# Performance work log

Measured on AMD Instinct MI355X. Metric: run time of the kernel, lower is better.

Reference implementation:

```python
import jax, jax.numpy as jnp
import numpy as np

N, E, D = 50000, 600000, 128

def _lin(key, fan_in, fan_out):
    kw, kb = jax.random.split(key)
    s = 1.0 / np.sqrt(fan_in)
    W = jax.random.uniform(kw, (fan_in, fan_out), minval=-s, maxval=s, dtype=jnp.float32)
    b = jax.random.uniform(kb, (fan_out,), minval=-s, maxval=s, dtype=jnp.float32)
    return W, b

def setup_inputs() -> dict:
    key = jax.random.key(0)
    ks = jax.random.split(key, 16)
    h = jax.random.normal(ks[0], (N, D), dtype=jnp.float32)
    pos = jax.random.normal(ks[1], (N, 2), dtype=jnp.float32)
    edge_index = jax.random.randint(ks[2], (2, E), 0, N, dtype=jnp.int64)
    edge_attr = jax.random.uniform(ks[3], (E, 1), dtype=jnp.float32)
    Wq, bq = _lin(ks[4], D, D)
    Wk, bk = _lin(ks[5], D, D)
    Wv, bv = _lin(ks[6], D, D)
    We1, be1 = _lin(ks[7], 1, D)
    We2, be2 = _lin(ks[8], D, D)
    Wa1, ba1 = _lin(ks[9], 3 * D, D)
    Wa2, ba2 = _lin(ks[10], D, 1)
    Wm1, bm1 = _lin(ks[11], 2 * D, D)
    Wm2, bm2 = _lin(ks[12], D, D)
    return dict(h=h, pos=pos, edge_index=edge_index, edge_attr=edge_attr,
                Wq=Wq, bq=bq, Wk=Wk, bk=bk, Wv=Wv, bv=bv,
                We1=We1, be1=be1, We2=We2, be2=be2,
                Wa1=Wa1, ba1=ba1, Wa2=Wa2, ba2=ba2,
                Wm1=Wm1, bm1=bm1, Wm2=Wm2, bm2=bm2)

def reference(h, pos, edge_index, edge_attr,
              Wq, bq, Wk, bk, Wv, bv,
              We1, be1, We2, be2,
              Wa1, ba1, Wa2, ba2,
              Wm1, bm1, Wm2, bm2):
    row, col = edge_index[0], edge_index[1]  # source, destination
    q = h @ Wq + bq                          # [N, D]
    k = h @ Wk + bk
    v = h @ Wv + bv
    e = jax.nn.relu(edge_attr @ We1 + be1) @ We2 + be2  # [E, D]
    # per-edge attention logits
    attn_in = jnp.concatenate([q[col], k[row], e], axis=-1)          # [E, 3D]
    logits = (jax.nn.relu(attn_in @ Wa1 + ba1) @ Wa2 + ba2)[:, 0]    # [E]
    # segment softmax grouped by destination node (torch_geometric style)
    seg_max = jax.ops.segment_max(logits, col, num_segments=N)       # [N]
    ex = jnp.exp(logits - seg_max[col])
    seg_sum = jax.ops.segment_sum(ex, col, num_segments=N)           # [N]
    w = ex / (seg_sum[col] + 1e-16)                                  # [E]
    # per-edge messages
    msg_in = jnp.concatenate([v[row], e], axis=-1)                   # [E, 2D]
    msg = jax.nn.silu(msg_in @ Wm1 + bm1) @ Wm2 + bm2                # [E, D]
    agg = jax.ops.segment_sum(msg * w[:, None], col, num_segments=N) # [N, D]
    return (h + agg, pos)
```

## Files before the change

### kernel.cpp

```cpp
#include <hip/hip_runtime.h>
#include <math.h>

#define D 128
#define RPB 32
#define SB 256

typedef __attribute__((ext_vector_type(8))) short bf16x8;
typedef __attribute__((ext_vector_type(4))) float f32x4;

__device__ inline unsigned f2bf(float f) {
    unsigned u = __float_as_uint(f);
    return (u + 0x7FFFu + ((u >> 16) & 1u)) >> 16;
}

__global__ __launch_bounds__(128) void prep(
    const float* __restrict__ Wq, const float* __restrict__ bq,
    const float* __restrict__ Wk, const float* __restrict__ bk,
    const float* __restrict__ Wv, const float* __restrict__ bv,
    const float* __restrict__ Wa1, const float* __restrict__ ba1,
    const float* __restrict__ Wm1, const float* __restrict__ bm1,
    const float* __restrict__ We1, const float* __restrict__ be1,
    const float* __restrict__ We2, const float* __restrict__ be2,
    ushort* __restrict__ Wpk,
    float* __restrict__ bqa, float* __restrict__ bka, float* __restrict__ bva,
    float* __restrict__ bounds,
    float2* __restrict__ AB, float2* __restrict__ MB,
    int* __restrict__ deg, int N)
{
    int b = blockIdx.x;
    int j = threadIdx.x;
    if (b < 384) {
        int which = b >> 7, i = b & 127;
        const float *A, *B;
        if (which == 0)      { A = Wq; B = Wa1; }
        else if (which == 1) { A = Wk; B = Wa1 + 128 * D; }
        else                 { A = Wv; B = Wm1; }
        float acc = 0.f;
        for (int k = 0; k < D; k++) acc += A[i * D + k] * B[k * D + j];
        int gc = which * 128 + j;
        int nt = gc >> 4;
        int ks = i >> 5;
        int lane = (((i >> 3) & 3) << 4) | (gc & 15);
        int j8 = i & 7;
        Wpk[((nt * 4 + ks) * 64 + lane) * 8 + j8] = (ushort)f2bf(acc);
    } else if (b < 387) {
        int which = b - 384;
        const float *bias, *B, *extra; float *out;
        if (which == 0)      { bias = bq; B = Wa1;           out = bqa; extra = ba1; }
        else if (which == 1) { bias = bk; B = Wa1 + 128 * D; out = bka; extra = nullptr; }
        else                 { bias = bv; B = Wm1;           out = bva; extra = bm1; }
        float acc = extra ? extra[j] : 0.f;
        for (int k = 0; k < D; k++) acc += bias[k] * B[k * D + j];
        out[j] = acc;
    } else if (b == 387) {
        __shared__ float sb[128];
        float w = We1[j], bb = be1[j];
        float t = (w != 0.f) ? (-bb / w) : 2.f;
        t = fminf(fmaxf(t, 0.f), 1.f);
        sb[j] = t;
        __syncthreads();
        for (int k = 2; k <= 128; k <<= 1)
            for (int jj = k >> 1; jj > 0; jj >>= 1) {
                int ixj = j ^ jj;
                if (ixj > j) {
                    float a = sb[j], c = sb[ixj];
                    bool up = ((j & k) == 0);
                    if (up ? (a > c) : (a < c)) { sb[j] = c; sb[ixj] = a; }
                }
                __syncthreads();
            }
        if (j == 0) { bounds[0] = 0.f; bounds[129] = 1.f; }
        bounds[1 + j] = sb[j];
    } else if (b < 517) {
        __shared__ float sb[128];
        __shared__ float Ae[128], Be[128];
        float w = We1[j], bb = be1[j];
        float t = (w != 0.f) ? (-bb / w) : 2.f;
        t = fminf(fmaxf(t, 0.f), 1.f);
        sb[j] = t;
        __syncthreads();
        for (int k = 2; k <= 128; k <<= 1)
            for (int jj = k >> 1; jj > 0; jj >>= 1) {
                int ixj = j ^ jj;
                if (ixj > j) {
                    float a = sb[j], c = sb[ixj];
                    bool up = ((j & k) == 0);
                    if (up ? (a > c) : (a < c)) { sb[j] = c; sb[ixj] = a; }
                }
                __syncthreads();
            }
        int i = b - 388;
        float lo = (i == 0)   ? 0.f : sb[i - 1];
        float hi = (i == 128) ? 1.f : sb[i];
        float m = 0.5f * (lo + hi);
        float ae = 0.f, be = 0.f;
        for (int k = 0; k < 128; k++) {
            float ww = We1[k], bb2 = be1[k];
            if (m * ww + bb2 > 0.f) { ae += ww * We2[k * D + j]; be += bb2 * We2[k * D + j]; }
        }
        be += be2[j];
        Ae[j] = ae; Be[j] = be;
        __syncthreads();
        float aa = 0.f, ba = 0.f, am = 0.f, bm = 0.f;
        for (int l = 0; l < 128; l++) {
            float ael = Ae[l], bel = Be[l];
            float wa = Wa1[(256 + l) * D + j];
            float wm = Wm1[(128 + l) * D + j];
            aa += ael * wa; ba += bel * wa;
            am += ael * wm; bm += bel * wm;
        }
        AB[i * 128 + j] = make_float2(aa, ba);
        MB[i * 128 + j] = make_float2(am, bm);
    } else {
        int i = (b - 517) * 128 + j;
        if (i < N) deg[i] = 0;
    }
}

__global__ __launch_bounds__(256) void node_gemm(
    const float* __restrict__ h, int N,
    const ushort* __restrict__ Wpk,
    const float* __restrict__ bqa, const float* __restrict__ bka, const float* __restrict__ bva,
    float* __restrict__ qa, unsigned* __restrict__ kv)
{
    __shared__ __align__(16) ushort hsb[64 * 128];
    int t = threadIdx.x;
    int row0 = blockIdx.x * 64;
#pragma unroll
    for (int i = 0; i < 4; i++) {
        int g = t + i * 256;
        int r = g >> 4, c = g & 15;
        int grow = row0 + r;
        float4 f0, f1;
        if (grow < N) {
            const float4* hp = (const float4*)(h + (size_t)grow * D + c * 8);
            f0 = hp[0]; f1 = hp[1];
        } else {
            f0 = make_float4(0.f, 0.f, 0.f, 0.f); f1 = f0;
        }
        ushort u[8] = { (ushort)f2bf(f0.x), (ushort)f2bf(f0.y), (ushort)f2bf(f0.z), (ushort)f2bf(f0.w),
                        (ushort)f2bf(f1.x), (ushort)f2bf(f1.y), (ushort)f2bf(f1.z), (ushort)f2bf(f1.w) };
        int pc = c ^ (r & 15);
        *(uint4*)&hsb[r * 128 + pc * 8] = *(uint4*)u;
    }
    __syncthreads();

    int w = t >> 6, l = t & 63;
    int lrow = w * 16 + (l & 15);
    f32x4 acc[24];
#pragma unroll
    for (int i = 0; i < 24; i++) acc[i] = (f32x4){0.f, 0.f, 0.f, 0.f};

    const bf16x8* WB = (const bf16x8*)Wpk;
#pragma unroll
    for (int ks = 0; ks < 4; ks++) {
        int c = (ks * 4 + (l >> 4)) ^ (l & 15);
        bf16x8 afrag = *(const bf16x8*)&hsb[lrow * 128 + c * 8];
#pragma unroll
        for (int nt = 0; nt < 24; nt++) {
            bf16x8 bfrag = WB[(nt * 4 + ks) * 64 + l];
            acc[nt] = __builtin_amdgcn_mfma_f32_16x16x32_bf16(afrag, bfrag, acc[nt], 0, 0, 0);
        }
    }

    int rbase = row0 + w * 16 + ((l >> 4) << 2);
    int cl = l & 15;
#pragma unroll
    for (int cc = 0; cc < 8; cc++) {
        float bqv = bqa[cc * 16 + cl];
        float bkv = bka[cc * 16 + cl];
        float bvv = bva[cc * 16 + cl];
        f32x4 aq = acc[cc], ak = acc[8 + cc], av = acc[16 + cc];
#pragma unroll
        for (int r = 0; r < 4; r++) {
            int row = rbase + r;
            if (row < N) {
                qa[(size_t)row * D + cc * 16 + cl] = aq[r] + bqv;
                kv[(size_t)row * D + cc * 16 + cl] =
                    (f2bf(av[r] + bvv) << 16) | f2bf(ak[r] + bkv);
            }
        }
    }
}

__global__ __launch_bounds__(256) void k_hist(const int* __restrict__ ei, int E,
                                              int* __restrict__ deg)
{
    int e = blockIdx.x * 256 + threadIdx.x;
    if (e < E) atomicAdd(deg + ei[E + e], 1);
}

__global__ __launch_bounds__(SB) void k_scan1(const int* __restrict__ deg, int N,
                                              int* __restrict__ partial)
{
    __shared__ int ls[SB];
    int t = threadIdx.x;
    int i = blockIdx.x * SB + t;
    ls[t] = (i < N) ? deg[i] : 0;
    __syncthreads();
    for (int s = SB / 2; s > 0; s >>= 1) {
        if (t < s) ls[t] += ls[t + s];
        __syncthreads();
    }
    if (t == 0) partial[blockIdx.x] = ls[0];
}

__global__ __launch_bounds__(SB) void k_scan23(const int* __restrict__ deg, int N,
                                               const int* __restrict__ partial, int NB,
                                               int* __restrict__ off)
{
    __shared__ int lp[SB];
    __shared__ int ls[SB];
    int t = threadIdx.x;
    int pv = (t < NB) ? partial[t] : 0;
    lp[t] = pv;
    __syncthreads();
    int pval = pv;
    for (int s = 1; s < SB; s <<= 1) {
        int add = (t >= s) ? lp[t - s] : 0;
        __syncthreads();
        pval += add;
        lp[t] = pval;
        __syncthreads();
    }
    int base = (blockIdx.x > 0) ? lp[blockIdx.x - 1] : 0;

    int i = blockIdx.x * SB + t;
    int v = (i < N) ? deg[i] : 0;
    ls[t] = v;
    __syncthreads();
    int val = v;
    for (int s = 1; s < SB; s <<= 1) {
        int add = (t >= s) ? ls[t - s] : 0;
        __syncthreads();
        val += add;
        ls[t] = val;
        __syncthreads();
    }
    if (i < N) off[i] = base + val - v;
}

__global__ __launch_bounds__(256) void k_scatter(const int* __restrict__ ei,
                                                 const float* __restrict__ eattr, int E,
                                                 const float* __restrict__ bounds,
                                                 int* __restrict__ off, int2* __restrict__ recs)
{
    __shared__ float b[130];
    int t = threadIdx.x;
    if (t < 130) b[t] = bounds[t];
    __syncthreads();
    int e = blockIdx.x * 256 + t;
    if (e >= E) return;
    int row = ei[e], col = ei[E + e];
    float a = eattr[e];
    int lo = 0, hi = 128;
    while (lo < hi) { int mid = (lo + hi + 1) >> 1; if (b[mid] <= a) lo = mid; else hi = mid - 1; }
    int p = atomicAdd(off + col, 1);
    recs[p] = make_int2(row | (lo << 17), __float_as_int(a));
}

__global__ __launch_bounds__(256) void node_all(
    const int2* __restrict__ recs, int N,
    const int* __restrict__ off,
    const float* __restrict__ qa, const unsigned* __restrict__ kv,
    const float2* __restrict__ AB, const float2* __restrict__ MB,
    const float* __restrict__ Wa2, const float* __restrict__ ba2,
    float* __restrict__ S, float* __restrict__ segsum)
{
    int t = threadIdx.x;
    int lane = t & 63, wv = t >> 6;
    int l = lane & 31;
    int n = blockIdx.x * 8 + wv * 2 + (lane >> 5);
    bool valid = (n < N);
    int start = 0, end = 0;
    if (valid) {
        end = off[n];
        start = (n > 0) ? off[n - 1] : 0;
    }

    const char* kvc = (const char*)kv;
    const char* ABc = (const char*)AB;
    const char* MBc = (const char*)MB;

    float4 q4 = valid ? *(const float4*)(qa + (size_t)n * D + 4 * l)
                      : make_float4(0.f, 0.f, 0.f, 0.f);
    float4 w4 = *(const float4*)(Wa2 + 4 * l);
    float ba2v = ba2[0];

    float m_run = -INFINITY;
    float a0 = 0.f, a1 = 0.f, a2 = 0.f, a3 = 0.f, ssum = 0.f;

    for (int idx = start; idx < end; idx++) {
        int2 rec = recs[idx];
        unsigned w0 = (unsigned)rec.x;
        float a = __int_as_float(rec.y);
        int rowb = (int)(w0 & 0x1FFFFu) << 9;
        int tabb = (int)(w0 >> 17) << 10;

        uint4 kvp = *(const uint4*)(kvc + rowb + (l << 4));
        float4 ab0 = *(const float4*)(ABc + tabb + (l << 5));
        float4 ab1 = *(const float4*)(ABc + tabb + (l << 5) + 16);
        float4 mb0 = *(const float4*)(MBc + tabb + (l << 5));
        float4 mb1 = *(const float4*)(MBc + tabb + (l << 5) + 16);

        float k0 = __uint_as_float(kvp.x << 16);
        float v0 = __uint_as_float(kvp.x & 0xFFFF0000u);
        float k1 = __uint_as_float(kvp.y << 16);
        float v1 = __uint_as_float(kvp.y & 0xFFFF0000u);
        float k2 = __uint_as_float(kvp.z << 16);
        float v2 = __uint_as_float(kvp.z & 0xFFFF0000u);
        float k3 = __uint_as_float(kvp.w << 16);
        float v3 = __uint_as_float(kvp.w & 0xFFFF0000u);

        float part = fmaxf(q4.x + k0 + a * ab0.x + ab0.y, 0.f) * w4.x
                   + fmaxf(q4.y + k1 + a * ab0.z + ab0.w, 0.f) * w4.y
                   + fmaxf(q4.z + k2 + a * ab1.x + ab1.y, 0.f) * w4.z
                   + fmaxf(q4.w + k3 + a * ab1.z + ab1.w, 0.f) * w4.w;
#pragma unroll
        for (int s = 1; s < 32; s <<= 1) part += __shfl_xor(part, s, 64);
        float lg = part + ba2v;

        float mN = fmaxf(m_run, lg);
        float sc = __expf(m_run - mN);
        float ex = __expf(lg - mN);
        m_run = mN;

        float x0 = v0 + a * mb0.x + mb0.y;
        float x1 = v1 + a * mb0.z + mb0.w;
        float x2 = v2 + a * mb1.x + mb1.y;
        float x3 = v3 + a * mb1.z + mb1.w;
        float s0 = x0 * __builtin_amdgcn_rcpf(1.f + __expf(-x0));
        float s1 = x1 * __builtin_amdgcn_rcpf(1.f + __expf(-x1));
        float s2 = x2 * __builtin_amdgcn_rcpf(1.f + __expf(-x2));
        float s3 = x3 * __builtin_amdgcn_rcpf(1.f + __expf(-x3));

        a0 = a0 * sc + ex * s0;
        a1 = a1 * sc + ex * s1;
        a2 = a2 * sc + ex * s2;
        a3 = a3 * sc + ex * s3;
        ssum = ssum * sc + ex;
    }

    if (valid) {
        float inv = __builtin_amdgcn_rcpf(ssum + 1e-16f);
        *(float4*)(S + (size_t)n * D + 4 * l) =
            make_float4(a0 * inv, a1 * inv, a2 * inv, a3 * inv);
        if (l == 0) segsum[n] = ssum;
    }
}

__global__ __launch_bounds__(256) void node_out(
    const float* __restrict__ h, int N,
    const float* __restrict__ S, const float* __restrict__ Wm2, const float* __restrict__ bm2,
    const float* __restrict__ segsum, float* __restrict__ out,
    const float* __restrict__ pos, int npos, int G1)
{
    int b = blockIdx.x;
    if (b >= G1) {
        int i = ((b - G1) * 256 + threadIdx.x) * 4;
        float* outp = out + (size_t)N * D;
        if (i + 3 < npos) {
            *(float4*)(outp + i) = *(const float4*)(pos + i);
        } else {
            for (int j = i; j < npos; j++) outp[j] = pos[j];
        }
        return;
    }
    __shared__ float hsT[D][36];
    int r0 = b * RPB;
    int t = threadIdx.x;
    for (int x = t; x < RPB * D; x += 256) {
        int r = x >> 7, cc = x & 127;
        hsT[cc][r] = (r0 + r < N) ? S[(size_t)(r0 + r) * D + cc] : 0.f;
    }
    __syncthreads();
    int c = t & 127, half = t >> 7;
    float acc[16];
#pragma unroll
    for (int r = 0; r < 16; r++) acc[r] = 0.f;
    for (int k = 0; k < D; k++) {
        float w = Wm2[k * D + c];
        const float4* hp = (const float4*)&hsT[k][half * 16];
#pragma unroll
        for (int p = 0; p < 4; p++) {
            float4 hv = hp[p];
            acc[p * 4 + 0] += hv.x * w;
            acc[p * 4 + 1] += hv.y * w;
            acc[p * 4 + 2] += hv.z * w;
            acc[p * 4 + 3] += hv.w * w;
        }
    }
    float bb = bm2[c];
#pragma unroll
    for (int r = 0; r < 16; r++) {
        int row = r0 + half * 16 + r;
        if (row < N) {
            float ws = segsum[row];
            ws = ws / (ws + 1e-16f);
            out[(size_t)row * D + c] = h[(size_t)row * D + c] + acc[r] + bb * ws;
        }
    }
}

extern "C" void kernel_launch(void* const* d_in, const int* in_sizes, int n_in,
                              void* d_out, int out_size, void* d_ws, size_t ws_size,
                              hipStream_t stream)
{
    const float* h     = (const float*)d_in[0];
    const float* pos   = (const float*)d_in[1];
    const int*   ei    = (const int*)d_in[2];
    const float* eattr = (const float*)d_in[3];
    const float* Wq  = (const float*)d_in[4];  const float* bq  = (const float*)d_in[5];
    const float* Wk  = (const float*)d_in[6];  const float* bk  = (const float*)d_in[7];
    const float* Wv  = (const float*)d_in[8];  const float* bv  = (const float*)d_in[9];
    const float* We1 = (const float*)d_in[10]; const float* be1 = (const float*)d_in[11];
    const float* We2 = (const float*)d_in[12]; const float* be2 = (const float*)d_in[13];
    const float* Wa1 = (const float*)d_in[14]; const float* ba1 = (const float*)d_in[15];
    const float* Wa2 = (const float*)d_in[16]; const float* ba2 = (const float*)d_in[17];
    const float* Wm1 = (const float*)d_in[18]; const float* bm1 = (const float*)d_in[19];
    const float* Wm2 = (const float*)d_in[20]; const float* bm2 = (const float*)d_in[21];

    int N = in_sizes[0] / D;
    int E = in_sizes[3];
    int NB = (N + SB - 1) / SB;

    float* ws = (float*)d_ws;
    size_t off_f = 0;
    auto alloc = [&](size_t n) { float* p = ws + off_f; off_f += (n + 63) & ~(size_t)63; return p; };

    ushort* Wpk = (ushort*)alloc(24 * 4 * 64 * 8 / 2);
    float* bqa = alloc(D); float* bka = alloc(D); float* bva = alloc(D);
    float* bounds = alloc(130);
    float2* AB = (float2*)alloc((size_t)129 * 128 * 2);
    float2* MB = (float2*)alloc((size_t)129 * 128 * 2);
    float* qa = alloc((size_t)N * D);
    unsigned* kv = (unsigned*)alloc((size_t)N * D);
    float* S  = qa;
    float* segsum = alloc(N);
    int* deg  = (int*)alloc(N);
    int* offs = (int*)alloc(N);
    int* partial = (int*)alloc(256);
    int2* recs = (int2*)alloc((size_t)E * 2);

    int G0 = 517 + (N + 127) / 128;
    prep<<<G0, 128, 0, stream>>>(Wq, bq, Wk, bk, Wv, bv, Wa1, ba1, Wm1, bm1,
                                 We1, be1, We2, be2,
                                 Wpk, bqa, bka, bva, bounds, AB, MB, deg, N);

    k_hist<<<(E + 255) / 256, 256, 0, stream>>>(ei, E, deg);
    k_scan1<<<NB, SB, 0, stream>>>(deg, N, partial);
    k_scan23<<<NB, SB, 0, stream>>>(deg, N, partial, NB, offs);
    k_scatter<<<(E + 255) / 256, 256, 0, stream>>>(ei, eattr, E, bounds, offs, recs);

    node_gemm<<<(N + 63) / 64, 256, 0, stream>>>(h, N, Wpk, bqa, bka, bva, qa, kv);

    node_all<<<(N + 7) / 8, 256, 0, stream>>>(recs, N, offs, qa, kv, AB, MB,
                                              Wa2, ba2, S, segsum);

    int G1 = (N + RPB - 1) / RPB;
    int G2 = (2 * N + 1023) / 1024;
    node_out<<<G1 + G2, 256, 0, stream>>>(h, N, S, Wm2, bm2, segsum, (float*)d_out,
                                          pos, 2 * N, G1);
}
```

Before: 299.5 us.

## Fuse launches, unroll edge loop by two, MFMA bf16 output GEMM

Folds the degree histogram into the prep kernel (memset replaces zeroing) and merges the scatter and node GEMM into one launch, cutting kernel launches and letting independent work overlap. The per-node edge loop now handles two edges per iteration, rescales the running softmax max only when a logit jumps by more than 8, and drops the constant ba2 bias, which cancels in the softmax. The aggregated messages are stored as bf16, and the final Wm2 projection moves from a scalar fp32 loop to MFMA bf16 with a prepacked weight. This trades some precision in the output GEMM for fewer launches and less memory traffic.

After: 253.8 us. 1.18x faster.

```diff
diff --git a/kernel.cpp b/kernel.cpp
--- a/kernel.cpp
+++ b/kernel.cpp
@@ -2,7 +2,6 @@
 #include <math.h>
 
 #define D 128
-#define RPB 32
 #define SB 256
 
 typedef __attribute__((ext_vector_type(8))) short bf16x8;
@@ -21,11 +20,13 @@
     const float* __restrict__ Wm1, const float* __restrict__ bm1,
     const float* __restrict__ We1, const float* __restrict__ be1,
     const float* __restrict__ We2, const float* __restrict__ be2,
-    ushort* __restrict__ Wpk,
+    const float* __restrict__ Wm2,
+    const int* __restrict__ ei, int E,
+    ushort* __restrict__ Wpk, ushort* __restrict__ Wpk2,
     float* __restrict__ bqa, float* __restrict__ bka, float* __restrict__ bva,
     float* __restrict__ bounds,
     float2* __restrict__ AB, float2* __restrict__ MB,
-    int* __restrict__ deg, int N)
+    int* __restrict__ deg)
 {
     int b = blockIdx.x;
     int j = threadIdx.x;
@@ -111,21 +112,98 @@
         }
         AB[i * 128 + j] = make_float2(aa, ba);
         MB[i * 128 + j] = make_float2(am, bm);
+    } else if (b < 645) {
+        int i = b - 517;
+        int nt = j >> 4;
+        int ks = i >> 5;
+        int lane = (((i >> 3) & 3) << 4) | (j & 15);
+        int j8 = i & 7;
+        Wpk2[((nt * 4 + ks) * 64 + lane) * 8 + j8] = (ushort)f2bf(Wm2[i * D + j]);
     } else {
-        int i = (b - 517) * 128 + j;
-        if (i < N) deg[i] = 0;
-    }
-}
-
-__global__ __launch_bounds__(256) void node_gemm(
+        int e = (b - 645) * 128 + j;
+        if (e < E) atomicAdd(deg + ei[E + e], 1);
+    }
+}
+
+__global__ __launch_bounds__(SB) void k_scan1(const int* __restrict__ deg, int N,
+                                              int* __restrict__ partial)
+{
+    __shared__ int ls[SB];
+    int t = threadIdx.x;
+    int i = blockIdx.x * SB + t;
+    ls[t] = (i < N) ? deg[i] : 0;
+    __syncthreads();
+    for (int s = SB / 2; s > 0; s >>= 1) {
+        if (t < s) ls[t] += ls[t + s];
+        __syncthreads();
+    }
+    if (t == 0) partial[blockIdx.x] = ls[0];
+}
+
+__global__ __launch_bounds__(SB) void k_scan23(const int* __restrict__ deg, int N,
+                                               const int* __restrict__ partial, int NB,
+                                               int* __restrict__ off)
+{
+    __shared__ int lp[SB];
+    __shared__ int ls[SB];
+    int t = threadIdx.x;
+    int pv = (t < NB) ? partial[t] : 0;
+    lp[t] = pv;
+    __syncthreads();
+    int pval = pv;
+    for (int s = 1; s < SB; s <<= 1) {
+        int add = (t >= s) ? lp[t - s] : 0;
+        __syncthreads();
+        pval += add;
+        lp[t] = pval;
+        __syncthreads();
+    }
+    int base = (blockIdx.x > 0) ? lp[blockIdx.x - 1] : 0;
+
+    int i = blockIdx.x * SB + t;
+    int v = (i < N) ? deg[i] : 0;
+    ls[t] = v;
+    __syncthreads();
+    int val = v;
+    for (int s = 1; s < SB; s <<= 1) {
+        int add = (t >= s) ? ls[t - s] : 0;
+        __syncthreads();
+        val += add;
+        ls[t] = val;
+        __syncthreads();
+    }
+    if (i < N) off[i] = base + val - v;
+}
+
+__global__ __launch_bounds__(256) void scatter_gemm(
+    const int* __restrict__ ei, const float* __restrict__ eattr, int E,
+    const float* __restrict__ bounds, int* __restrict__ off, int2* __restrict__ recs,
+    int GS,
     const float* __restrict__ h, int N,
     const ushort* __restrict__ Wpk,
     const float* __restrict__ bqa, const float* __restrict__ bka, const float* __restrict__ bva,
     float* __restrict__ qa, unsigned* __restrict__ kv)
 {
     __shared__ __align__(16) ushort hsb[64 * 128];
+    __shared__ float bnd[130];
     int t = threadIdx.x;
-    int row0 = blockIdx.x * 64;
+    int blk = blockIdx.x;
+
+    if (blk < GS) {
+        if (t < 130) bnd[t] = bounds[t];
+        __syncthreads();
+        int e = blk * 256 + t;
+        if (e >= E) return;
+        int row = ei[e], col = ei[E + e];
+        float a = eattr[e];
+        int lo = 0, hi = 128;
+        while (lo < hi) { int mid = (lo + hi + 1) >> 1; if (bnd[mid] <= a) lo = mid; else hi = mid - 1; }
+        int p = atomicAdd(off + col, 1);
+        recs[p] = make_int2(row | (lo << 17), __float_as_int(a));
+        return;
+    }
+
+    int row0 = (blk - GS) * 64;
 #pragma unroll
     for (int i = 0; i < 4; i++) {
         int g = t + i * 256;
@@ -183,94 +261,17 @@
     }
 }
 
-__global__ __launch_bounds__(256) void k_hist(const int* __restrict__ ei, int E,
-                                              int* __restrict__ deg)
-{
-    int e = blockIdx.x * 256 + threadIdx.x;
-    if (e < E) atomicAdd(deg + ei[E + e], 1);
-}
-
-__global__ __launch_bounds__(SB) void k_scan1(const int* __restrict__ deg, int N,
-                                              int* __restrict__ partial)
-{
-    __shared__ int ls[SB];
-    int t = threadIdx.x;
-    int i = blockIdx.x * SB + t;
-    ls[t] = (i < N) ? deg[i] : 0;
-    __syncthreads();
-    for (int s = SB / 2; s > 0; s >>= 1) {
-        if (t < s) ls[t] += ls[t + s];
-        __syncthreads();
-    }
-    if (t == 0) partial[blockIdx.x] = ls[0];
-}
-
-__global__ __launch_bounds__(SB) void k_scan23(const int* __restrict__ deg, int N,
-                                               const int* __restrict__ partial, int NB,
-                                               int* __restrict__ off)
-{
-    __shared__ int lp[SB];
-    __shared__ int ls[SB];
-    int t = threadIdx.x;
-    int pv = (t < NB) ? partial[t] : 0;
-    lp[t] = pv;
-    __syncthreads();
-    int pval = pv;
-    for (int s = 1; s < SB; s <<= 1) {
-        int add = (t >= s) ? lp[t - s] : 0;
-        __syncthreads();
-        pval += add;
-        lp[t] = pval;
-        __syncthreads();
-    }
-    int base = (blockIdx.x > 0) ? lp[blockIdx.x - 1] : 0;
-
-    int i = blockIdx.x * SB + t;
-    int v = (i < N) ? deg[i] : 0;
-    ls[t] = v;
-    __syncthreads();
-    int val = v;
-    for (int s = 1; s < SB; s <<= 1) {
-        int add = (t >= s) ? ls[t - s] : 0;
-        __syncthreads();
-        val += add;
-        ls[t] = val;
-        __syncthreads();
-    }
-    if (i < N) off[i] = base + val - v;
-}
-
-__global__ __launch_bounds__(256) void k_scatter(const int* __restrict__ ei,
-                                                 const float* __restrict__ eattr, int E,
-                                                 const float* __restrict__ bounds,
-                                                 int* __restrict__ off, int2* __restrict__ recs)
-{
-    __shared__ float b[130];
-    int t = threadIdx.x;
-    if (t < 130) b[t] = bounds[t];
-    __syncthreads();
-    int e = blockIdx.x * 256 + t;
-    if (e >= E) return;
-    int row = ei[e], col = ei[E + e];
-    float a = eattr[e];
-    int lo = 0, hi = 128;
-    while (lo < hi) { int mid = (lo + hi + 1) >> 1; if (b[mid] <= a) lo = mid; else hi = mid - 1; }
-    int p = atomicAdd(off + col, 1);
-    recs[p] = make_int2(row | (lo << 17), __float_as_int(a));
-}
-
 __global__ __launch_bounds__(256) void node_all(
     const int2* __restrict__ recs, int N,
     const int* __restrict__ off,
     const float* __restrict__ qa, const unsigned* __restrict__ kv,
     const float2* __restrict__ AB, const float2* __restrict__ MB,
-    const float* __restrict__ Wa2, const float* __restrict__ ba2,
-    float* __restrict__ S, float* __restrict__ segsum)
+    const float* __restrict__ Wa2,
+    unsigned* __restrict__ Sb, float* __restrict__ segsum)
 {
     int t = threadIdx.x;
-    int lane = t & 63, wv = t >> 6;
-    int l = lane & 31;
-    int n = blockIdx.x * 8 + wv * 2 + (lane >> 5);
+    int l = t & 31;
+    int n = blockIdx.x * 8 + (t >> 5);
     bool valid = (n < N);
     int start = 0, end = 0;
     if (valid) {
@@ -285,79 +286,129 @@
     float4 q4 = valid ? *(const float4*)(qa + (size_t)n * D + 4 * l)
                       : make_float4(0.f, 0.f, 0.f, 0.f);
     float4 w4 = *(const float4*)(Wa2 + 4 * l);
-    float ba2v = ba2[0];
 
     float m_run = -INFINITY;
     float a0 = 0.f, a1 = 0.f, a2 = 0.f, a3 = 0.f, ssum = 0.f;
 
-    for (int idx = start; idx < end; idx++) {
+    int idx = start;
+    for (; idx + 2 <= end; idx += 2) {
+        int2 rec1 = recs[idx];
+        int2 rec2 = recs[idx + 1];
+        unsigned u1 = (unsigned)rec1.x, u2 = (unsigned)rec2.x;
+        float at1 = __int_as_float(rec1.y), at2 = __int_as_float(rec2.y);
+        int rb1 = (int)(u1 & 0x1FFFFu) << 9, tb1 = (int)(u1 >> 17) << 10;
+        int rb2 = (int)(u2 & 0x1FFFFu) << 9, tb2 = (int)(u2 >> 17) << 10;
+
+        uint4 kp1 = *(const uint4*)(kvc + rb1 + (l << 4));
+        uint4 kp2 = *(const uint4*)(kvc + rb2 + (l << 4));
+        float4 ab0a = *(const float4*)(ABc + tb1 + (l << 5));
+        float4 ab1a = *(const float4*)(ABc + tb1 + (l << 5) + 16);
+        float4 mb0a = *(const float4*)(MBc + tb1 + (l << 5));
+        float4 mb1a = *(const float4*)(MBc + tb1 + (l << 5) + 16);
+        float4 ab0b = *(const float4*)(ABc + tb2 + (l << 5));
+        float4 ab1b = *(const float4*)(ABc + tb2 + (l << 5) + 16);
+        float4 mb0b = *(const float4*)(MBc + tb2 + (l << 5));
+        float4 mb1b = *(const float4*)(MBc + tb2 + (l << 5) + 16);
+
+        float p1 = fmaxf(q4.x + __uint_as_float(kp1.x << 16) + at1 * ab0a.x + ab0a.y, 0.f) * w4.x
+                 + fmaxf(q4.y + __uint_as_float(kp1.y << 16) + at1 * ab0a.z + ab0a.w, 0.f) * w4.y
+                 + fmaxf(q4.z + __uint_as_float(kp1.z << 16) + at1 * ab1a.x + ab1a.y, 0.f) * w4.z
+                 + fmaxf(q4.w + __uint_as_float(kp1.w << 16) + at1 * ab1a.z + ab1a.w, 0.f) * w4.w;
+        float p2 = fmaxf(q4.x + __uint_as_float(kp2.x << 16) + at2 * ab0b.x + ab0b.y, 0.f) * w4.x
+                 + fmaxf(q4.y + __uint_as_float(kp2.y << 16) + at2 * ab0b.z + ab0b.w, 0.f) * w4.y
+                 + fmaxf(q4.z + __uint_as_float(kp2.z << 16) + at2 * ab1b.x + ab1b.y, 0.f) * w4.z
+                 + fmaxf(q4.w + __uint_as_float(kp2.w << 16) + at2 * ab1b.z + ab1b.w, 0.f) * w4.w;
+#pragma unroll
+        for (int s = 1; s < 32; s <<= 1) {
+            p1 += __shfl_xor(p1, s, 64);
+            p2 += __shfl_xor(p2, s, 64);
+        }
+        float d1 = p1 - m_run, d2 = p2 - m_run;
+        if (fmaxf(d1, d2) > 8.f) {
+            float mN = fmaxf(fmaxf(p1, p2), m_run);
+            float sc = __expf(m_run - mN);
+            a0 *= sc; a1 *= sc; a2 *= sc; a3 *= sc; ssum *= sc;
+            m_run = mN; d1 = p1 - mN; d2 = p2 - mN;
+        }
+        float ex1 = __expf(d1), ex2 = __expf(d2);
+
+        float x0 = __uint_as_float(kp1.x & 0xFFFF0000u) + at1 * mb0a.x + mb0a.y;
+        float x1 = __uint_as_float(kp1.y & 0xFFFF0000u) + at1 * mb0a.z + mb0a.w;
+        float x2 = __uint_as_float(kp1.z & 0xFFFF0000u) + at1 * mb1a.x + mb1a.y;
+        float x3 = __uint_as_float(kp1.w & 0xFFFF0000u) + at1 * mb1a.z + mb1a.w;
+        float y0 = __uint_as_float(kp2.x & 0xFFFF0000u) + at2 * mb0b.x + mb0b.y;
+        float y1 = __uint_as_float(kp2.y & 0xFFFF0000u) + at2 * mb0b.z + mb0b.w;
+        float y2 = __uint_as_float(kp2.z & 0xFFFF0000u) + at2 * mb1b.x + mb1b.y;
+        float y3 = __uint_as_float(kp2.w & 0xFFFF0000u) + at2 * mb1b.z + mb1b.w;
+        float s10 = x0 * __builtin_amdgcn_rcpf(1.f + __expf(-x0));
+        float s11 = x1 * __builtin_amdgcn_rcpf(1.f + __expf(-x1));
+        float s12 = x2 * __builtin_amdgcn_rcpf(1.f + __expf(-x2));
+        float s13 = x3 * __builtin_amdgcn_rcpf(1.f + __expf(-x3));
+        float s20 = y0 * __builtin_amdgcn_rcpf(1.f + __expf(-y0));
+        float s21 = y1 * __builtin_amdgcn_rcpf(1.f + __expf(-y1));
+        float s22 = y2 * __builtin_amdgcn_rcpf(1.f + __expf(-y2));
+        float s23 = y3 * __builtin_amdgcn_rcpf(1.f + __expf(-y3));
+
+        a0 = fmaf(ex2, s20, fmaf(ex1, s10, a0));
+        a1 = fmaf(ex2, s21, fmaf(ex1, s11, a1));
+        a2 = fmaf(ex2, s22, fmaf(ex1, s12, a2));
+        a3 = fmaf(ex2, s23, fmaf(ex1, s13, a3));
+        ssum += ex1 + ex2;
+    }
+    if (idx < end) {
         int2 rec = recs[idx];
-        unsigned w0 = (unsigned)rec.x;
+        unsigned u1 = (unsigned)rec.x;
         float a = __int_as_float(rec.y);
-        int rowb = (int)(w0 & 0x1FFFFu) << 9;
-        int tabb = (int)(w0 >> 17) << 10;
-
-        uint4 kvp = *(const uint4*)(kvc + rowb + (l << 4));
-        float4 ab0 = *(const float4*)(ABc + tabb + (l << 5));
-        float4 ab1 = *(const float4*)(ABc + tabb + (l << 5) + 16);
-        float4 mb0 = *(const float4*)(MBc + tabb + (l << 5));
-        float4 mb1 = *(const float4*)(MBc + tabb + (l << 5) + 16);
-
-        float k0 = __uint_as_float(kvp.x << 16);
-        float v0 = __uint_as_float(kvp.x & 0xFFFF0000u);
-        float k1 = __uint_as_float(kvp.y << 16);
-        float v1 = __uint_as_float(kvp.y & 0xFFFF0000u);
-        float k2 = __uint_as_float(kvp.z << 16);
-        float v2 = __uint_as_float(kvp.z & 0xFFFF0000u);
-        float k3 = __uint_as_float(kvp.w << 16);
-        float v3 = __uint_as_float(kvp.w & 0xFFFF0000u);
-
-        float part = fmaxf(q4.x + k0 + a * ab0.x + ab0.y, 0.f) * w4.x
-                   + fmaxf(q4.y + k1 + a * ab0.z + ab0.w, 0.f) * w4.y
-                   + fmaxf(q4.z + k2 + a * ab1.x + ab1.y, 0.f) * w4.z
-                   + fmaxf(q4.w + k3 + a * ab1.z + ab1.w, 0.f) * w4.w;
-#pragma unroll
-        for (int s = 1; s < 32; s <<= 1) part += __shfl_xor(part, s, 64);
-        float lg = part + ba2v;
-
-        float mN = fmaxf(m_run, lg);
-        float sc = __expf(m_run - mN);
-        float ex = __expf(lg - mN);
-        m_run = mN;
-
-        float x0 = v0 + a * mb0.x + mb0.y;
-        float x1 = v1 + a * mb0.z + mb0.w;
-        float x2 = v2 + a * mb1.x + mb1.y;
-        float x3 = v3 + a * mb1.z + mb1.w;
-        float s0 = x0 * __builtin_amdgcn_rcpf(1.f + __expf(-x0));
-        float s1 = x1 * __builtin_amdgcn_rcpf(1.f + __expf(-x1));
-        float s2 = x2 * __builtin_amdgcn_rcpf(1.f + __expf(-x2));
-        float s3 = x3 * __builtin_amdgcn_rcpf(1.f + __expf(-x3));
-
-        a0 = a0 * sc + ex * s0;
-        a1 = a1 * sc + ex * s1;
-        a2 = a2 * sc + ex * s2;
-        a3 = a3 * sc + ex * s3;
-        ssum = ssum * sc + ex;
+        int rb = (int)(u1 & 0x1FFFFu) << 9, tb = (int)(u1 >> 17) << 10;
+        uint4 kp = *(const uint4*)(kvc + rb + (l << 4));
+        float4 ab0 = *(const float4*)(ABc + tb + (l << 5));
+        float4 ab1 = *(const float4*)(ABc + tb + (l << 5) + 16);
+        float4 mb0 = *(const float4*)(MBc + tb + (l << 5));
+        float4 mb1 = *(const float4*)(MBc + tb + (l << 5) + 16);
+        float p1 = fmaxf(q4.x + __uint_as_float(kp.x << 16) + a * ab0.x + ab0.y, 0.f) * w4.x
+                 + fmaxf(q4.y + __uint_as_float(kp.y << 16) + a * ab0.z + ab0.w, 0.f) * w4.y
+                 + fmaxf(q4.z + __uint_as_float(kp.z << 16) + a * ab1.x + ab1.y, 0.f) * w4.z
+                 + fmaxf(q4.w + __uint_as_float(kp.w << 16) + a * ab1.z + ab1.w, 0.f) * w4.w;
+#pragma unroll
+        for (int s = 1; s < 32; s <<= 1) p1 += __shfl_xor(p1, s, 64);
+        float d1 = p1 - m_run;
+        if (d1 > 8.f) {
+            float mN = p1;
+            float sc = __expf(m_run - mN);
+            a0 *= sc; a1 *= sc; a2 *= sc; a3 *= sc; ssum *= sc;
+            m_run = mN; d1 = 0.f;
+        }
+        float ex = __expf(d1);
+        float x0 = __uint_as_float(kp.x & 0xFFFF0000u) + a * mb0.x + mb0.y;
+        float x1 = __uint_as_float(kp.y & 0xFFFF0000u) + a * mb0.z + mb0.w;
+        float x2 = __uint_as_float(kp.z & 0xFFFF0000u) + a * mb1.x + mb1.y;
+        float x3 = __uint_as_float(kp.w & 0xFFFF0000u) + a * mb1.z + mb1.w;
+        a0 = fmaf(ex, x0 * __builtin_amdgcn_rcpf(1.f + __expf(-x0)), a0);
+        a1 = fmaf(ex, x1 * __builtin_amdgcn_rcpf(1.f + __expf(-x1)), a1);
+        a2 = fmaf(ex, x2 * __builtin_amdgcn_rcpf(1.f + __expf(-x2)), a2);
+        a3 = fmaf(ex, x3 * __builtin_amdgcn_rcpf(1.f + __expf(-x3)), a3);
+        ssum += ex;
     }
 
     if (valid) {
         float inv = __builtin_amdgcn_rcpf(ssum + 1e-16f);
-        *(float4*)(S + (size_t)n * D + 4 * l) =
-            make_float4(a0 * inv, a1 * inv, a2 * inv, a3 * inv);
+        unsigned pw0 = f2bf(a0 * inv) | (f2bf(a1 * inv) << 16);
+        unsigned pw1 = f2bf(a2 * inv) | (f2bf(a3 * inv) << 16);
+        *(uint2*)(Sb + (size_t)n * 64 + 2 * l) = make_uint2(pw0, pw1);
         if (l == 0) segsum[n] = ssum;
     }
 }
 
 __global__ __launch_bounds__(256) void node_out(
     const float* __restrict__ h, int N,
-    const float* __restrict__ S, const float* __restrict__ Wm2, const float* __restrict__ bm2,
-    const float* __restrict__ segsum, float* __restrict__ out,
-    const float* __restrict__ pos, int npos, int G1)
+    const unsigned* __restrict__ Sb, const ushort* __restrict__ Wpk2,
+    const float* __restrict__ bm2, const float* __restrict__ segsum,
+    float* __restrict__ out, const float* __restrict__ pos, int npos, int G1)
 {
     int b = blockIdx.x;
+    int t = threadIdx.x;
     if (b >= G1) {
-        int i = ((b - G1) * 256 + threadIdx.x) * 4;
+        int i = ((b - G1) * 256 + t) * 4;
         float* outp = out + (size_t)N * D;
         if (i + 3 < npos) {
             *(float4*)(outp + i) = *(const float4*)(pos + i);
@@ -366,38 +417,53 @@
         }
         return;
     }
-    __shared__ float hsT[D][36];
-    int r0 = b * RPB;
-    int t = threadIdx.x;
-    for (int x = t; x < RPB * D; x += 256) {
-        int r = x >> 7, cc = x & 127;
-        hsT[cc][r] = (r0 + r < N) ? S[(size_t)(r0 + r) * D + cc] : 0.f;
+    __shared__ __align__(16) ushort ssb[64 * 128];
+    int row0 = b * 64;
+#pragma unroll
+    for (int i = 0; i < 4; i++) {
+        int g = t + i * 256;
+        int r = g >> 4, c = g & 15;
+        int grow = row0 + r;
+        uint4 u = make_uint4(0u, 0u, 0u, 0u);
+        if (grow < N) u = *(const uint4*)(Sb + (size_t)grow * 64 + c * 4);
+        int pc = c ^ (r & 15);
+        *(uint4*)&ssb[r * 128 + pc * 8] = u;
     }
     __syncthreads();
-    int c = t & 127, half = t >> 7;
-    float acc[16];
-#pragma unroll
-    for (int r = 0; r < 16; r++) acc[r] = 0.f;
-    for (int k = 0; k < D; k++) {
-        float w = Wm2[k * D + c];
-        const float4* hp = (const float4*)&hsT[k][half * 16];
-#pragma unroll
-        for (int p = 0; p < 4; p++) {
-            float4 hv = hp[p];
-            acc[p * 4 + 0] += hv.x * w;
-            acc[p * 4 + 1] += hv.y * w;
-            acc[p * 4 + 2] += hv.z * w;
-            acc[p * 4 + 3] += hv.w * w;
-        }
-    }
-    float bb = bm2[c];
-#pragma unroll
-    for (int r = 0; r < 16; r++) {
-        int row = r0 + half * 16 + r;
-        if (row < N) {
-            float ws = segsum[row];
-            ws = ws / (ws + 1e-16f);
-            out[(size_t)row * D + c] = h[(size_t)row * D + c] + acc[r] + bb * ws;
+
+    int w = t >> 6, l = t & 63;
+    int lrow = w * 16 + (l & 15);
+    f32x4 acc[8];
+#pragma unroll
+    for (int i = 0; i < 8; i++) acc[i] = (f32x4){0.f, 0.f, 0.f, 0.f};
+
+    const bf16x8* WB = (const bf16x8*)Wpk2;
+#pragma unroll
+    for (int ks = 0; ks < 4; ks++) {
+        int c = (ks * 4 + (l >> 4)) ^ (l & 15);
+        bf16x8 afrag = *(const bf16x8*)&ssb[lrow * 128 + c * 8];
+#pragma unroll
+        for (int nt = 0; nt < 8; nt++) {
+            bf16x8 bfrag = WB[(nt * 4 + ks) * 64 + l];
+            acc[nt] = __builtin_amdgcn_mfma_f32_16x16x32_bf16(afrag, bfrag, acc[nt], 0, 0, 0);
+        }
+    }
+
+    int rbase = row0 + w * 16 + ((l >> 4) << 2);
+    int cl = l & 15;
+#pragma unroll
+    for (int cc = 0; cc < 8; cc++) {
+        float bb = bm2[cc * 16 + cl];
+        f32x4 av = acc[cc];
+#pragma unroll
+        for (int r = 0; r < 4; r++) {
+            int row = rbase + r;
+            if (row < N) {
+                float ws_ = segsum[row];
+                ws_ = ws_ / (ws_ + 1e-16f);
+                out[(size_t)row * D + cc * 16 + cl] =
+                    h[(size_t)row * D + cc * 16 + cl] + av[r] + bb * ws_;
+            }
         }
     }
 }
@@ -416,7 +482,7 @@
     const float* We1 = (const float*)d_in[10]; const float* be1 = (const float*)d_in[11];
     const float* We2 = (const float*)d_in[12]; const float* be2 = (const float*)d_in[13];
     const float* Wa1 = (const float*)d_in[14]; const float* ba1 = (const float*)d_in[15];
-    const float* Wa2 = (const float*)d_in[16]; const float* ba2 = (const float*)d_in[17];
+    const float* Wa2 = (const float*)d_in[16];
     const float* Wm1 = (const float*)d_in[18]; const float* bm1 = (const float*)d_in[19];
     const float* Wm2 = (const float*)d_in[20]; const float* bm2 = (const float*)d_in[21];
 
@@ -428,37 +494,41 @@
     size_t off_f = 0;
     auto alloc = [&](size_t n) { float* p = ws + off_f; off_f += (n + 63) & ~(size_t)63; return p; };
 
-    ushort* Wpk = (ushort*)alloc(24 * 4 * 64 * 8 / 2);
+    ushort* Wpk  = (ushort*)alloc(24 * 4 * 64 * 8 / 2);
+    ushort* Wpk2 = (ushort*)alloc(8 * 4 * 64 * 8 / 2);
     float* bqa = alloc(D); float* bka = alloc(D); float* bva = alloc(D);
     float* bounds = alloc(130);
     float2* AB = (float2*)alloc((size_t)129 * 128 * 2);
     float2* MB = (float2*)alloc((size_t)129 * 128 * 2);
     float* qa = alloc((size_t)N * D);
     unsigned* kv = (unsigned*)alloc((size_t)N * D);
-    float* S  = qa;
+    unsigned* Sb = (unsigned*)alloc((size_t)N * 64);
     float* segsum = alloc(N);
     int* deg  = (int*)alloc(N);
     int* offs = (int*)alloc(N);
     int* partial = (int*)alloc(256);
     int2* recs = (int2*)alloc((size_t)E * 2);
 
-    int G0 = 517 + (N + 127) / 128;
-    prep<<<G0, 128, 0, stream>>>(Wq, bq, Wk, bk, Wv, bv, Wa1, ba1, Wm1, bm1,
-                                 We1, be1, We2, be2,
-                                 Wpk, bqa, bka, bva, bounds, AB, MB, deg, N);
-
-    k_hist<<<(E + 255) / 256, 256, 0, stream>>>(ei, E, deg);
+    hipMemsetAsync(deg, 0, (size_t)N * 4, stream);
+
+    int HB = (E + 127) / 128;
+    prep<<<645 + HB, 128, 0, stream>>>(Wq, bq, Wk, bk, Wv, bv, Wa1, ba1, Wm1, bm1,
+                                       We1, be1, We2, be2, Wm2, ei, E,
+                                       Wpk, Wpk2, bqa, bka, bva, bounds, AB, MB, deg);
+
     k_scan1<<<NB, SB, 0, stream>>>(deg, N, partial);
     k_scan23<<<NB, SB, 0, stream>>>(deg, N, partial, NB, offs);
-    k_scatter<<<(E + 255) / 256, 256, 0, stream>>>(ei, eattr, E, bounds, offs, recs);
-
-    node_gemm<<<(N + 63) / 64, 256, 0, stream>>>(h, N, Wpk, bqa, bka, bva, qa, kv);
-
-    node_all<<<(N + 7) / 8, 256, 0, stream>>>(recs, N, offs, qa, kv, AB, MB,
-                                              Wa2, ba2, S, segsum);
-
-    int G1 = (N + RPB - 1) / RPB;
+
+    int GS = (E + 255) / 256;
+    int GG = (N + 63) / 64;
+    scatter_gemm<<<GS + GG, 256, 0, stream>>>(ei, eattr, E, bounds, offs, recs, GS,
+                                              h, N, Wpk, bqa, bka, bva, qa, kv);
+
+    node_all<<<(N + 7) / 8, 256, 0, stream>>>(recs, N, offs, qa, kv, AB, MB, Wa2,
+                                              Sb, segsum);
+
+    int G1 = (N + 63) / 64;
     int G2 = (2 * N + 1023) / 1024;
-    node_out<<<G1 + G2, 256, 0, stream>>>(h, N, S, Wm2, bm2, segsum, (float*)d_out,
+    node_out<<<G1 + G2, 256, 0, stream>>>(h, N, Sb, Wpk2, bm2, segsum, (float*)d_out,
                                           pos, 2 * N, G1);
 }
```
